# Kernel optimization log

Hardware: AMD Instinct MI355X
Metric: run time of the kernel (lower is better)

The kernel has to match this reference:

```python
import jax, jax.numpy as jnp
import numpy as np

EPS = 1e-5
SLOPE = 0.2
DIMS = [128, 32, 64, 32, 16, 8, 4, 2]  # widths before final Linear(2,1)


def _layernorm(h, g, b):
    m = jnp.mean(h, axis=-1, keepdims=True)
    v = jnp.mean(jnp.square(h - m), axis=-1, keepdims=True)
    return (h - m) * jax.lax.rsqrt(v + EPS) * g + b


def setup_inputs() -> dict:
    key = jax.random.key(0)
    ks = jax.random.split(key, 2 * len(DIMS) + 2)
    inp = {"x": jax.random.normal(ks[0], (524288, DIMS[0]), dtype=jnp.float32)}
    # 7 bias-free Linears, each followed by LayerNorm(gamma, beta)
    for i in range(7):
        din, dout = DIMS[i], DIMS[i + 1]
        inp[f"W{i+1}"] = jax.random.normal(ks[2 * i + 1], (din, dout), dtype=jnp.float32) / np.sqrt(din)
        inp[f"g{i+1}"] = jnp.ones((dout,), dtype=jnp.float32)
        inp[f"bt{i+1}"] = jnp.zeros((dout,), dtype=jnp.float32)
    # final Linear(2 -> 1) with bias
    inp["W8"] = jax.random.normal(ks[-1], (2, 1), dtype=jnp.float32) / np.sqrt(2.0)
    inp["b8"] = jnp.zeros((1,), dtype=jnp.float32)
    return inp


def reference(x, W1, g1, bt1, W2, g2, bt2, W3, g3, bt3, W4, g4, bt4,
              W5, g5, bt5, W6, g6, bt6, W7, g7, bt7, W8, b8):
    Ws = [W1, W2, W3, W4, W5, W6, W7]
    gs = [g1, g2, g3, g4, g5, g6, g7]
    bs = [bt1, bt2, bt3, bt4, bt5, bt6, bt7]
    h = x
    for W, g, b in zip(Ws, gs, bs):
        h = jnp.dot(h, W)                 # Linear, bias=False
        h = _layernorm(h, g, b)           # LayerNorm
        h = jnp.where(h > 0, h, SLOPE * h)  # LeakyReLU(0.2)
    return jnp.dot(h, W8) + b8            # final Linear(2, 1)
```

## Files before the change

kernel.cpp:

```cpp
#include <hip/hip_runtime.h>

#define EPS 1e-5f
#define SLOPE 0.2f

typedef float v2f __attribute__((ext_vector_type(2)));

__device__ __forceinline__ v2f pkfma(float s, v2f w, v2f a) {
  v2f sv = {s, s};
  return __builtin_elementwise_fma(sv, w, a);
}

template<int N2>
__device__ __forceinline__ void ln_lrelu_pk(v2f* h, const float* __restrict__ g,
                                            const float* __restrict__ b) {
  const v2f* g2 = reinterpret_cast<const v2f*>(g);
  const v2f* b2 = reinterpret_cast<const v2f*>(b);
  const float invN = 1.0f / (2 * N2);
  float m, vv;
  if constexpr (N2 >= 2) {
    v2f s0 = {0.f, 0.f}, s1 = {0.f, 0.f};
#pragma unroll
    for (int j = 0; j < N2; j += 2) { s0 += h[j]; s1 += h[j + 1]; }
    v2f st = s0 + s1;
    m = (st.x + st.y) * invN;
    v2f q0 = {0.f, 0.f}, q1 = {0.f, 0.f};
#pragma unroll
    for (int j = 0; j < N2; j += 2) {
      v2f d0 = h[j] - m, d1 = h[j + 1] - m;
      q0 = __builtin_elementwise_fma(d0, d0, q0);
      q1 = __builtin_elementwise_fma(d1, d1, q1);
    }
    v2f qt = q0 + q1;
    vv = (qt.x + qt.y) * invN;
  } else {
    m = (h[0].x + h[0].y) * 0.5f;
    float dx = h[0].x - m, dy = h[0].y - m;
    vv = (dx * dx + dy * dy) * 0.5f;
  }
  const float rs = rsqrtf(vv + EPS);
#pragma unroll
  for (int j = 0; j < N2; ++j) {
    v2f t = (h[j] - m) * rs * g2[j] + b2[j];
    h[j] = __builtin_elementwise_max(t, SLOPE * t);
  }
}

template<int DIN, int DOUT2>
__device__ __forceinline__ void linear_pk(const v2f* hin, v2f* hout,
                                          const float* __restrict__ W) {
#pragma unroll
  for (int j = 0; j < DOUT2; ++j) hout[j] = (v2f){0.f, 0.f};
#pragma unroll
  for (int k = 0; k < DIN; ++k) {
    float hk = (k & 1) ? hin[k >> 1].y : hin[k >> 1].x;
    const v2f* wr = reinterpret_cast<const v2f*>(W + k * (DOUT2 * 2));
#pragma unroll
    for (int j = 0; j < DOUT2; ++j) hout[j] = pkfma(hk, wr[j], hout[j]);
  }
}

__global__ __launch_bounds__(256) void disc_fused(
    const float* __restrict__ x,
    const float* __restrict__ W1, const float* __restrict__ g1, const float* __restrict__ b1,
    const float* __restrict__ W2, const float* __restrict__ g2, const float* __restrict__ b2,
    const float* __restrict__ W3, const float* __restrict__ g3, const float* __restrict__ b3,
    const float* __restrict__ W4, const float* __restrict__ g4, const float* __restrict__ b4,
    const float* __restrict__ W5, const float* __restrict__ g5, const float* __restrict__ b5,
    const float* __restrict__ W6, const float* __restrict__ g6, const float* __restrict__ b6,
    const float* __restrict__ W7, const float* __restrict__ g7, const float* __restrict__ b7,
    const float* __restrict__ W8, const float* __restrict__ b8,
    float* __restrict__ out, int nrows) {
  const long row = (long)blockIdx.x * 256 + threadIdx.x;
  if (row >= (long)nrows) return;

  const float4* __restrict__ xr4 = reinterpret_cast<const float4*>(x) + row * 32;
  v2f h1[16];
#pragma unroll
  for (int j = 0; j < 16; ++j) h1[j] = (v2f){0.f, 0.f};

#pragma unroll
  for (int cc = 0; cc < 4; ++cc) {
    float4 bv[8];
#pragma unroll
    for (int q = 0; q < 8; ++q) bv[q] = xr4[cc * 8 + q];
#pragma unroll
    for (int q = 0; q < 8; ++q) {
#pragma unroll
      for (int kk = 0; kk < 4; ++kk) {
        float xk = (kk == 0) ? bv[q].x : (kk == 1) ? bv[q].y
                 : (kk == 2) ? bv[q].z : bv[q].w;
        const v2f* wr =
            reinterpret_cast<const v2f*>(W1 + (cc * 32 + q * 4 + kk) * 32);
#pragma unroll
        for (int j = 0; j < 16; ++j) h1[j] = pkfma(xk, wr[j], h1[j]);
      }
    }
  }
  ln_lrelu_pk<16>(h1, g1, b1);

  const v2f* W2v = reinterpret_cast<const v2f*>(W2);

  float sum2 = 0.f, sq2 = 0.f;
#pragma unroll 1
  for (int jb = 0; jb < 16; ++jb) {
    v2f a01 = {0.f, 0.f}, a23 = {0.f, 0.f};
#pragma unroll
    for (int k = 0; k < 32; ++k) {
      float hk = (k & 1) ? h1[k >> 1].y : h1[k >> 1].x;
      a01 = pkfma(hk, W2v[k * 32 + jb * 2], a01);
      a23 = pkfma(hk, W2v[k * 32 + jb * 2 + 1], a23);
    }
    sum2 += (a01.x + a01.y) + (a23.x + a23.y);
    sq2 = fmaf(a01.x, a01.x, sq2); sq2 = fmaf(a01.y, a01.y, sq2);
    sq2 = fmaf(a23.x, a23.x, sq2); sq2 = fmaf(a23.y, a23.y, sq2);
  }
  const float m2 = sum2 * (1.0f / 64.0f);
  const float v2 = fmaf(-m2, m2, sq2 * (1.0f / 64.0f));
  const float rs2 = rsqrtf(v2 + EPS);

  v2f h3[16];
#pragma unroll
  for (int i = 0; i < 16; ++i) h3[i] = (v2f){0.f, 0.f};
#pragma unroll 1
  for (int jb = 0; jb < 16; ++jb) {
    v2f a01 = {0.f, 0.f}, a23 = {0.f, 0.f};
#pragma unroll
    for (int k = 0; k < 32; ++k) {
      float hk = (k & 1) ? h1[k >> 1].y : h1[k >> 1].x;
      a01 = pkfma(hk, W2v[k * 32 + jb * 2], a01);
      a23 = pkfma(hk, W2v[k * 32 + jb * 2 + 1], a23);
    }
#pragma unroll
    for (int u = 0; u < 4; ++u) {
      float a = (u == 0) ? a01.x : (u == 1) ? a01.y : (u == 2) ? a23.x : a23.y;
      int j = jb * 4 + u;
      float y = (a - m2) * rs2 * g2[j] + b2[j];
      y = fmaxf(y, SLOPE * y);
      const v2f* wr3 = reinterpret_cast<const v2f*>(W3 + j * 32);
#pragma unroll
      for (int i = 0; i < 16; ++i) h3[i] = pkfma(y, wr3[i], h3[i]);
    }
  }
  ln_lrelu_pk<16>(h3, g3, b3);

  v2f h4[8]; linear_pk<32, 8>(h3, h4, W4); ln_lrelu_pk<8>(h4, g4, b4);
  v2f h5[4]; linear_pk<16, 4>(h4, h5, W5); ln_lrelu_pk<4>(h5, g5, b5);
  v2f h6[2]; linear_pk<8, 2>(h5, h6, W6);  ln_lrelu_pk<2>(h6, g6, b6);
  v2f h7[1]; linear_pk<4, 1>(h6, h7, W7);  ln_lrelu_pk<1>(h7, g7, b7);

  out[row] = fmaf(h7[0].y, W8[1], fmaf(h7[0].x, W8[0], b8[0]));
}

extern "C" void kernel_launch(void* const* d_in, const int* in_sizes, int n_in,
                              void* d_out, int out_size, void* d_ws, size_t ws_size,
                              hipStream_t stream) {
  const float* x  = (const float*)d_in[0];
  const float* W1 = (const float*)d_in[1];
  const float* g1 = (const float*)d_in[2];
  const float* b1 = (const float*)d_in[3];
  const float* W2 = (const float*)d_in[4];
  const float* g2 = (const float*)d_in[5];
  const float* b2 = (const float*)d_in[6];
  const float* W3 = (const float*)d_in[7];
  const float* g3 = (const float*)d_in[8];
  const float* b3 = (const float*)d_in[9];
  const float* W4 = (const float*)d_in[10];
  const float* g4 = (const float*)d_in[11];
  const float* b4 = (const float*)d_in[12];
  const float* W5 = (const float*)d_in[13];
  const float* g5 = (const float*)d_in[14];
  const float* b5 = (const float*)d_in[15];
  const float* W6 = (const float*)d_in[16];
  const float* g6 = (const float*)d_in[17];
  const float* b6 = (const float*)d_in[18];
  const float* W7 = (const float*)d_in[19];
  const float* g7 = (const float*)d_in[20];
  const float* b7 = (const float*)d_in[21];
  const float* W8 = (const float*)d_in[22];
  const float* b8 = (const float*)d_in[23];
  float* out = (float*)d_out;

  const int nrows = in_sizes[0] / 128;
  const int grid = (nrows + 255) / 256;
  hipLaunchKernelGGL(disc_fused, dim3(grid), dim3(256), 0, stream,
                     x, W1, g1, b1, W2, g2, b2, W3, g3, b3, W4, g4, b4,
                     W5, g5, b5, W6, g6, b6, W7, g7, b7, W8, b8, out, nrows);
}
```

Measured before the change: 169.2 us.

## Split fused MLP into layer-1 kernel and remaining-layers kernel via workspace

Splits the single fused kernel into two launches. The first computes Linear1+LayerNorm+LeakyReLU and writes the 32-wide activations to the workspace. The second reads them back and runs the remaining layers. The layer-1 chunk loop is also set to not unroll. The aim is lower register pressure per kernel for better occupancy and latency hiding, at the cost of an extra 64MB write and read round trip plus a second launch. It falls back to the fused kernel when the workspace is too small.

```diff
diff --git a/kernel.cpp b/kernel.cpp
--- a/kernel.cpp
+++ b/kernel.cpp
@@ -57,6 +57,133 @@
 #pragma unroll
     for (int j = 0; j < DOUT2; ++j) hout[j] = pkfma(hk, wr[j], hout[j]);
   }
+}
+
+__device__ __forceinline__ void layer1_body(const float4* __restrict__ xr4,
+                                            const float* __restrict__ W1,
+                                            const float* __restrict__ g1,
+                                            const float* __restrict__ b1,
+                                            v2f* h1) {
+#pragma unroll
+  for (int j = 0; j < 16; ++j) h1[j] = (v2f){0.f, 0.f};
+#pragma unroll 1
+  for (int cc = 0; cc < 4; ++cc) {
+    float4 bv[8];
+#pragma unroll
+    for (int q = 0; q < 8; ++q) bv[q] = xr4[cc * 8 + q];
+#pragma unroll
+    for (int q = 0; q < 8; ++q) {
+#pragma unroll
+      for (int kk = 0; kk < 4; ++kk) {
+        float xk = (kk == 0) ? bv[q].x : (kk == 1) ? bv[q].y
+                 : (kk == 2) ? bv[q].z : bv[q].w;
+        const v2f* wr =
+            reinterpret_cast<const v2f*>(W1 + (cc * 32 + q * 4 + kk) * 32);
+#pragma unroll
+        for (int j = 0; j < 16; ++j) h1[j] = pkfma(xk, wr[j], h1[j]);
+      }
+    }
+  }
+  ln_lrelu_pk<16>(h1, g1, b1);
+}
+
+__device__ __forceinline__ float rest_body(
+    v2f* h1,
+    const float* __restrict__ W2, const float* __restrict__ g2, const float* __restrict__ b2,
+    const float* __restrict__ W3, const float* __restrict__ g3, const float* __restrict__ b3,
+    const float* __restrict__ W4, const float* __restrict__ g4, const float* __restrict__ b4,
+    const float* __restrict__ W5, const float* __restrict__ g5, const float* __restrict__ b5,
+    const float* __restrict__ W6, const float* __restrict__ g6, const float* __restrict__ b6,
+    const float* __restrict__ W7, const float* __restrict__ g7, const float* __restrict__ b7,
+    const float* __restrict__ W8, const float* __restrict__ b8) {
+  const v2f* W2v = reinterpret_cast<const v2f*>(W2);
+
+  float sum2 = 0.f, sq2 = 0.f;
+#pragma unroll 1
+  for (int jb = 0; jb < 16; ++jb) {
+    v2f a01 = {0.f, 0.f}, a23 = {0.f, 0.f};
+#pragma unroll
+    for (int k = 0; k < 32; ++k) {
+      float hk = (k & 1) ? h1[k >> 1].y : h1[k >> 1].x;
+      a01 = pkfma(hk, W2v[k * 32 + jb * 2], a01);
+      a23 = pkfma(hk, W2v[k * 32 + jb * 2 + 1], a23);
+    }
+    sum2 += (a01.x + a01.y) + (a23.x + a23.y);
+    sq2 = fmaf(a01.x, a01.x, sq2); sq2 = fmaf(a01.y, a01.y, sq2);
+    sq2 = fmaf(a23.x, a23.x, sq2); sq2 = fmaf(a23.y, a23.y, sq2);
+  }
+  const float m2 = sum2 * (1.0f / 64.0f);
+  const float v2 = fmaf(-m2, m2, sq2 * (1.0f / 64.0f));
+  const float rs2 = rsqrtf(v2 + EPS);
+
+  v2f h3[16];
+#pragma unroll
+  for (int i = 0; i < 16; ++i) h3[i] = (v2f){0.f, 0.f};
+#pragma unroll 1
+  for (int jb = 0; jb < 16; ++jb) {
+    v2f a01 = {0.f, 0.f}, a23 = {0.f, 0.f};
+#pragma unroll
+    for (int k = 0; k < 32; ++k) {
+      float hk = (k & 1) ? h1[k >> 1].y : h1[k >> 1].x;
+      a01 = pkfma(hk, W2v[k * 32 + jb * 2], a01);
+      a23 = pkfma(hk, W2v[k * 32 + jb * 2 + 1], a23);
+    }
+#pragma unroll
+    for (int u = 0; u < 4; ++u) {
+      float a = (u == 0) ? a01.x : (u == 1) ? a01.y : (u == 2) ? a23.x : a23.y;
+      int j = jb * 4 + u;
+      float y = (a - m2) * rs2 * g2[j] + b2[j];
+      y = fmaxf(y, SLOPE * y);
+      const v2f* wr3 = reinterpret_cast<const v2f*>(W3 + j * 32);
+#pragma unroll
+      for (int i = 0; i < 16; ++i) h3[i] = pkfma(y, wr3[i], h3[i]);
+    }
+  }
+  ln_lrelu_pk<16>(h3, g3, b3);
+
+  v2f h4[8]; linear_pk<32, 8>(h3, h4, W4); ln_lrelu_pk<8>(h4, g4, b4);
+  v2f h5[4]; linear_pk<16, 4>(h4, h5, W5); ln_lrelu_pk<4>(h5, g5, b5);
+  v2f h6[2]; linear_pk<8, 2>(h5, h6, W6);  ln_lrelu_pk<2>(h6, g6, b6);
+  v2f h7[1]; linear_pk<4, 1>(h6, h7, W7);  ln_lrelu_pk<1>(h7, g7, b7);
+
+  return fmaf(h7[0].y, W8[1], fmaf(h7[0].x, W8[0], b8[0]));
+}
+
+__global__ __launch_bounds__(256) void l1_kernel(
+    const float* __restrict__ x,
+    const float* __restrict__ W1, const float* __restrict__ g1,
+    const float* __restrict__ b1,
+    float* __restrict__ h1out, int nrows) {
+  const long row = (long)blockIdx.x * 256 + threadIdx.x;
+  if (row >= (long)nrows) return;
+  const float4* __restrict__ xr4 = reinterpret_cast<const float4*>(x) + row * 32;
+  v2f h1[16];
+  layer1_body(xr4, W1, g1, b1, h1);
+  float4* __restrict__ o4 = reinterpret_cast<float4*>(h1out) + row * 8;
+  const float4* h14 = reinterpret_cast<const float4*>(h1);
+#pragma unroll
+  for (int i = 0; i < 8; ++i) o4[i] = h14[i];
+}
+
+__global__ __launch_bounds__(256) void rest_kernel(
+    const float* __restrict__ h1in,
+    const float* __restrict__ W2, const float* __restrict__ g2, const float* __restrict__ b2,
+    const float* __restrict__ W3, const float* __restrict__ g3, const float* __restrict__ b3,
+    const float* __restrict__ W4, const float* __restrict__ g4, const float* __restrict__ b4,
+    const float* __restrict__ W5, const float* __restrict__ g5, const float* __restrict__ b5,
+    const float* __restrict__ W6, const float* __restrict__ g6, const float* __restrict__ b6,
+    const float* __restrict__ W7, const float* __restrict__ g7, const float* __restrict__ b7,
+    const float* __restrict__ W8, const float* __restrict__ b8,
+    float* __restrict__ out, int nrows) {
+  const long row = (long)blockIdx.x * 256 + threadIdx.x;
+  if (row >= (long)nrows) return;
+  v2f h1[16];
+  const float4* i4 = reinterpret_cast<const float4*>(h1in) + row * 8;
+  float4* h14 = reinterpret_cast<float4*>(h1);
+#pragma unroll
+  for (int i = 0; i < 8; ++i) h14[i] = i4[i];
+  out[row] = rest_body(h1, W2, g2, b2, W3, g3, b3, W4, g4, b4,
+                       W5, g5, b5, W6, g6, b6, W7, g7, b7, W8, b8);
 }
 
 __global__ __launch_bounds__(256) void disc_fused(
@@ -72,83 +199,11 @@
     float* __restrict__ out, int nrows) {
   const long row = (long)blockIdx.x * 256 + threadIdx.x;
   if (row >= (long)nrows) return;
-
   const float4* __restrict__ xr4 = reinterpret_cast<const float4*>(x) + row * 32;
   v2f h1[16];
-#pragma unroll
-  for (int j = 0; j < 16; ++j) h1[j] = (v2f){0.f, 0.f};
-
-#pragma unroll
-  for (int cc = 0; cc < 4; ++cc) {
-    float4 bv[8];
-#pragma unroll
-    for (int q = 0; q < 8; ++q) bv[q] = xr4[cc * 8 + q];
-#pragma unroll
-    for (int q = 0; q < 8; ++q) {
-#pragma unroll
-      for (int kk = 0; kk < 4; ++kk) {
-        float xk = (kk == 0) ? bv[q].x : (kk == 1) ? bv[q].y
-                 : (kk == 2) ? bv[q].z : bv[q].w;
-        const v2f* wr =
-            reinterpret_cast<const v2f*>(W1 + (cc * 32 + q * 4 + kk) * 32);
-#pragma unroll
-        for (int j = 0; j < 16; ++j) h1[j] = pkfma(xk, wr[j], h1[j]);
-      }
-    }
-  }
-  ln_lrelu_pk<16>(h1, g1, b1);
-
-  const v2f* W2v = reinterpret_cast<const v2f*>(W2);
-
-  float sum2 = 0.f, sq2 = 0.f;
-#pragma unroll 1
-  for (int jb = 0; jb < 16; ++jb) {
-    v2f a01 = {0.f, 0.f}, a23 = {0.f, 0.f};
-#pragma unroll
-    for (int k = 0; k < 32; ++k) {
-      float hk = (k & 1) ? h1[k >> 1].y : h1[k >> 1].x;
-      a01 = pkfma(hk, W2v[k * 32 + jb * 2], a01);
-      a23 = pkfma(hk, W2v[k * 32 + jb * 2 + 1], a23);
-    }
-    sum2 += (a01.x + a01.y) + (a23.x + a23.y);
-    sq2 = fmaf(a01.x, a01.x, sq2); sq2 = fmaf(a01.y, a01.y, sq2);
-    sq2 = fmaf(a23.x, a23.x, sq2); sq2 = fmaf(a23.y, a23.y, sq2);
-  }
-  const float m2 = sum2 * (1.0f / 64.0f);
-  const float v2 = fmaf(-m2, m2, sq2 * (1.0f / 64.0f));
-  const float rs2 = rsqrtf(v2 + EPS);
-
-  v2f h3[16];
-#pragma unroll
-  for (int i = 0; i < 16; ++i) h3[i] = (v2f){0.f, 0.f};
-#pragma unroll 1
-  for (int jb = 0; jb < 16; ++jb) {
-    v2f a01 = {0.f, 0.f}, a23 = {0.f, 0.f};
-#pragma unroll
-    for (int k = 0; k < 32; ++k) {
-      float hk = (k & 1) ? h1[k >> 1].y : h1[k >> 1].x;
-      a01 = pkfma(hk, W2v[k * 32 + jb * 2], a01);
-      a23 = pkfma(hk, W2v[k * 32 + jb * 2 + 1], a23);
-    }
-#pragma unroll
-    for (int u = 0; u < 4; ++u) {
-      float a = (u == 0) ? a01.x : (u == 1) ? a01.y : (u == 2) ? a23.x : a23.y;
-      int j = jb * 4 + u;
-      float y = (a - m2) * rs2 * g2[j] + b2[j];
-      y = fmaxf(y, SLOPE * y);
-      const v2f* wr3 = reinterpret_cast<const v2f*>(W3 + j * 32);
-#pragma unroll
-      for (int i = 0; i < 16; ++i) h3[i] = pkfma(y, wr3[i], h3[i]);
-    }
-  }
-  ln_lrelu_pk<16>(h3, g3, b3);
-
-  v2f h4[8]; linear_pk<32, 8>(h3, h4, W4); ln_lrelu_pk<8>(h4, g4, b4);
-  v2f h5[4]; linear_pk<16, 4>(h4, h5, W5); ln_lrelu_pk<4>(h5, g5, b5);
-  v2f h6[2]; linear_pk<8, 2>(h5, h6, W6);  ln_lrelu_pk<2>(h6, g6, b6);
-  v2f h7[1]; linear_pk<4, 1>(h6, h7, W7);  ln_lrelu_pk<1>(h7, g7, b7);
-
-  out[row] = fmaf(h7[0].y, W8[1], fmaf(h7[0].x, W8[0], b8[0]));
+  layer1_body(xr4, W1, g1, b1, h1);
+  out[row] = rest_body(h1, W2, g2, b2, W3, g3, b3, W4, g4, b4,
+                       W5, g5, b5, W6, g6, b6, W7, g7, b7, W8, b8);
 }
 
 extern "C" void kernel_launch(void* const* d_in, const int* in_sizes, int n_in,
@@ -182,7 +237,18 @@
 
   const int nrows = in_sizes[0] / 128;
   const int grid = (nrows + 255) / 256;
-  hipLaunchKernelGGL(disc_fused, dim3(grid), dim3(256), 0, stream,
-                     x, W1, g1, b1, W2, g2, b2, W3, g3, b3, W4, g4, b4,
-                     W5, g5, b5, W6, g6, b6, W7, g7, b7, W8, b8, out, nrows);
-}
+  const size_t need = (size_t)nrows * 32 * sizeof(float);
+
+  if (ws_size >= need) {
+    float* h1buf = (float*)d_ws;
+    hipLaunchKernelGGL(l1_kernel, dim3(grid), dim3(256), 0, stream,
+                       x, W1, g1, b1, h1buf, nrows);
+    hipLaunchKernelGGL(rest_kernel, dim3(grid), dim3(256), 0, stream,
+                       h1buf, W2, g2, b2, W3, g3, b3, W4, g4, b4,
+                       W5, g5, b5, W6, g6, b6, W7, g7, b7, W8, b8, out, nrows);
+  } else {
+    hipLaunchKernelGGL(disc_fused, dim3(grid), dim3(256), 0, stream,
+                       x, W1, g1, b1, W2, g2, b2, W3, g3, b3, W4, g4, b4,
+                       W5, g5, b5, W6, g6, b6, W7, g7, b7, W8, b8, out, nrows);
+  }
+}
```

New measurement: 192.9 us. 14.0% more time.
